# Kernel optimization log

Measured on AMD Instinct MI355X. Metric: run time of the kernel, lower is better.

## Reference

```python
import jax, jax.numpy as jnp
import numpy as np
import math

B, T, D, H = 2, 2048, 1024, 16
DH = D // H          # 64
NB = DH // 2         # 32 rope blocks
EPS = 1e-5


def _layernorm(x, g, b):
    m = jnp.mean(x, axis=-1, keepdims=True)
    v = jnp.var(x, axis=-1, keepdims=True)
    return (x - m) * jax.lax.rsqrt(v + EPS) * g + b


def _rope(x, cos, sin):
    # x: (B,H,T,DH); cos/sin: (B,H,T,NB)
    x1 = x[..., 0::2]
    x2 = x[..., 1::2]
    o1 = x1 * cos - x2 * sin
    o2 = x1 * sin + x2 * cos
    return jnp.stack([o1, o2], axis=-1).reshape(x.shape)


def setup_inputs() -> dict:
    key = jax.random.key(0)
    ks = jax.random.split(key, 16)
    x = jax.random.normal(ks[0], (B, T, D), dtype=jnp.float32)
    # genuine RoPE angles broadcast to (B,H,T,NB)
    inv_freq = 1.0 / (10000.0 ** (np.arange(NB, dtype=np.float32) / NB))
    ang = jnp.asarray(np.arange(T, dtype=np.float32)[:, None] * inv_freq[None, :])  # (T,NB)
    cos_a = jnp.broadcast_to(jnp.cos(ang)[None, None], (B, H, T, NB)).astype(jnp.float32)
    sin_a = jnp.broadcast_to(jnp.sin(ang)[None, None], (B, H, T, NB)).astype(jnp.float32)
    causal_mask = jnp.triu(jnp.ones((T, T), dtype=bool), k=1)  # True above diagonal -> masked
    s = 0.02
    def w(k, shp):
        return jax.random.normal(k, shp, dtype=jnp.float32) * s
    return {
        "x": x, "cos_a": cos_a, "sin_a": sin_a, "causal_mask": causal_mask,
        "Wq": w(ks[1], (D, D)), "bq": jnp.zeros((D,), jnp.float32),
        "Wk": w(ks[2], (D, D)), "bk": jnp.zeros((D,), jnp.float32),
        "Wv": w(ks[3], (D, D)), "bv": jnp.zeros((D,), jnp.float32),
        "Wo": w(ks[4], (D, D)), "bo": jnp.zeros((D,), jnp.float32),
        "g1": jnp.ones((D,), jnp.float32), "b1n": jnp.zeros((D,), jnp.float32),
        "g2": jnp.ones((D,), jnp.float32), "b2n": jnp.zeros((D,), jnp.float32),
        "W1": w(ks[5], (D, 4 * D)), "bf1": jnp.zeros((4 * D,), jnp.float32),
        "W2": w(ks[6], (4 * D, D)), "bf2": jnp.zeros((D,), jnp.float32),
    }


def reference(x, cos_a, sin_a, causal_mask, Wq, bq, Wk, bk, Wv, bv, Wo, bo,
              g1, b1n, g2, b2n, W1, bf1, W2, bf2):
    h = _layernorm(x, g1, b1n)
    def heads(y):
        return y.reshape(B, T, H, DH).transpose(0, 2, 1, 3)  # (B,H,T,DH)
    Q = heads(h @ Wq + bq)
    K = heads(h @ Wk + bk)
    V = heads(h @ Wv + bv)
    Q = _rope(Q, cos_a, sin_a)
    K = _rope(K, cos_a, sin_a)
    scale = math.sqrt(DH)
    scores = jnp.einsum('bhqd,bhkd->bhqk', Q, K) / scale
    scores = jnp.where(causal_mask[None, None], -jnp.inf, scores)
    attn = jax.nn.softmax(scores, axis=-1)
    out = jnp.einsum('bhqk,bhkd->bhqd', attn, V)
    out = out.transpose(0, 2, 1, 3).reshape(B, T, D)
    out = out @ Wo + bo
    x = x + out  # dropout=0.0 (eval)
    h2 = _layernorm(x, g2, b2n)
    ffn = jax.nn.gelu(h2 @ W1 + bf1, approximate=False) @ W2 + bf2
    return x + ffn
```

## Files before the change

### kernel.cpp

```cpp
#include <hip/hip_runtime.h>

typedef unsigned short u16;
typedef unsigned int   u32;
typedef __attribute__((ext_vector_type(8))) short          short8;
typedef __attribute__((ext_vector_type(4))) float          f32x4;
typedef __attribute__((ext_vector_type(8))) unsigned short u16x8;
typedef __attribute__((ext_vector_type(4))) unsigned short u16x4;

#define T_SEQ  2048
#define DMODEL 1024
#define NHEAD  16
#define DHEAD  64
#define HBUF   4194304

__device__ __forceinline__ float bf2f(u16 u) {
    u32 i = ((u32)u) << 16; float f; __builtin_memcpy(&f, &i, 4); return f;
}
__device__ __forceinline__ u16 f2bf(float f) {
    u32 x; __builtin_memcpy(&x, &f, 4);
    return (u16)((x + 0x7FFFu + ((x >> 16) & 1u)) >> 16);
}

__device__ __forceinline__ void gld16(const u16* g, u16* l) {
    auto gp = reinterpret_cast<const __attribute__((address_space(1))) u32*>(
        reinterpret_cast<uintptr_t>(g));
    auto lp = reinterpret_cast<__attribute__((address_space(3))) u32*>(
        (u32)reinterpret_cast<uintptr_t>(l));
    __builtin_amdgcn_global_load_lds(gp, lp, 16, 0, 0);
}

__global__ __launch_bounds__(256) void ln_k(const float* __restrict__ x,
                                            const float* __restrict__ g,
                                            const float* __restrict__ bb,
                                            u16* __restrict__ out)
{
    int row = blockIdx.x, tid = threadIdx.x;
    const float* xr = x + (size_t)row * DMODEL;
    f32x4 v = *(const f32x4*)(xr + tid * 4);
    float s  = v[0] + v[1] + v[2] + v[3];
    float s2 = v[0]*v[0] + v[1]*v[1] + v[2]*v[2] + v[3]*v[3];
    #pragma unroll
    for (int o = 32; o; o >>= 1) { s += __shfl_xor(s, o); s2 += __shfl_xor(s2, o); }
    __shared__ float rs[4], rq[4];
    if ((tid & 63) == 0) { rs[tid >> 6] = s; rq[tid >> 6] = s2; }
    __syncthreads();
    float S  = rs[0] + rs[1] + rs[2] + rs[3];
    float S2 = rq[0] + rq[1] + rq[2] + rq[3];
    float mean = S * (1.f / DMODEL);
    float var  = S2 * (1.f / DMODEL) - mean * mean;
    float rstd = rsqrtf(var + 1e-5f);
    f32x4 gv = *(const f32x4*)(g + tid * 4);
    f32x4 bv = *(const f32x4*)(bb + tid * 4);
    u16x4 o;
    #pragma unroll
    for (int e = 0; e < 4; e++)
        o[e] = f2bf((v[e] - mean) * rstd * gv[e] + bv[e]);
    *(u16x4*)(out + (size_t)row * DMODEL + tid * 4) = o;
}

__device__ __forceinline__ void tr_body(const float* __restrict__ in,
                                        u16* __restrict__ out, int R, int C,
                                        int bx, int by, int tid)
{
    __shared__ u16 s[64][72];
    int c0 = bx * 64, r0 = by * 64;
    #pragma unroll
    for (int p = 0; p < 2; p++) {
        int r = (tid >> 3) + p * 32, cq = (tid & 7) * 8;
        const float* ip = in + (size_t)(r0 + r) * C + c0 + cq;
        f32x4 a = *(const f32x4*)ip;
        f32x4 b = *(const f32x4*)(ip + 4);
        u16x8 o;
        #pragma unroll
        for (int e = 0; e < 4; e++) { o[e] = f2bf(a[e]); o[4 + e] = f2bf(b[e]); }
        *(u16x8*)(&s[r][cq]) = o;
    }
    __syncthreads();
    int oc = tid >> 2, kq = (tid & 3) * 16;
    u16 tmp[16] __attribute__((aligned(16)));
    #pragma unroll
    for (int e = 0; e < 16; e++) tmp[e] = s[kq + e][oc];
    u16* op = out + (size_t)(c0 + oc) * R + r0 + kq;
    *(u16x8*)op       = *(const u16x8*)(&tmp[0]);
    *(u16x8*)(op + 8) = *(const u16x8*)(&tmp[8]);
}

__global__ __launch_bounds__(256) void trall_k(const float* __restrict__ w0, const float* __restrict__ w1,
                                               const float* __restrict__ w2, const float* __restrict__ w3,
                                               const float* __restrict__ wf1, const float* __restrict__ wf2,
                                               u16* __restrict__ o0, u16* __restrict__ o1,
                                               u16* __restrict__ o2, u16* __restrict__ o3,
                                               u16* __restrict__ of1, u16* __restrict__ of2)
{
    int z = blockIdx.z;
    if (z < 4) {
        const float* in = (z == 0) ? w0 : (z == 1) ? w1 : (z == 2) ? w2 : w3;
        u16* out        = (z == 0) ? o0 : (z == 1) ? o1 : (z == 2) ? o2 : o3;
        tr_body(in, out, 1024, 1024, blockIdx.x, blockIdx.y, threadIdx.x);
    } else if (z < 8) {
        tr_body(wf1, of1, 1024, 4096, blockIdx.x + 16 * (z - 4), blockIdx.y, threadIdx.x);
    } else {
        tr_body(wf2, of2, 4096, 1024, blockIdx.x, blockIdx.y + 16 * (z - 8), threadIdx.x);
    }
}

constexpr int EPI_QKV = 0, EPI_RESF = 1, EPI_GELU = 2, EPI_RES2 = 3;

template<int EPI, int BM>
__global__ __launch_bounds__(256) void gemm_k(
    const u16* __restrict__ A, const u16* __restrict__ Bt, void* __restrict__ outv,
    int M, int N, int K, int Kld,
    const float* __restrict__ b0, const float* __restrict__ b1, const float* __restrict__ b2,
    const float* __restrict__ resid,
    const float* __restrict__ cosp, const float* __restrict__ sinp)
{
    constexpr int MI = BM / 32;
    constexpr int ASZ = BM * 32, BSZ = 128 * 32;
    __shared__ u16 As[2 * ASZ];
    __shared__ u16 Bs[2 * BSZ];
    int tid = threadIdx.x;
    int n0 = blockIdx.x * 128, m0 = blockIdx.y * BM;
    int wave = tid >> 6, lane = tid & 63, lm = lane & 15, ko = lane >> 4;
    int wm = (wave & 1) * (BM / 2), wn = (wave >> 1) * 64;
    f32x4 acc[MI][4];
    #pragma unroll
    for (int i = 0; i < MI; i++)
        #pragma unroll
        for (int j = 0; j < 4; j++) acc[i][j] = (f32x4){0.f, 0.f, 0.f, 0.f};

    int srow = wave * 16 + (lane >> 2);
    int scol = (lane & 3) * 8;
    const u16* Ag = A  + (size_t)(m0 + srow) * Kld + scol;
    const u16* Bg = Bt + (size_t)(n0 + srow) * Kld + scol;
    u16* Al = &As[wave * 16 * 32];
    u16* Bl = &Bs[wave * 16 * 32];

    gld16(Ag, Al);
    if constexpr (BM == 128) gld16(Ag + 64 * (size_t)Kld, Al + 64 * 32);
    gld16(Bg,                    Bl);
    gld16(Bg + 64 * (size_t)Kld, Bl + 64 * 32);

    int t = 0;
    for (int kt = 0; kt < K; kt += 32, t ^= 1) {
        __syncthreads();
        if (kt + 32 < K) {
            u16* Al2 = Al + (t ^ 1) * ASZ;
            u16* Bl2 = Bl + (t ^ 1) * BSZ;
            gld16(Ag + 32, Al2);
            if constexpr (BM == 128) gld16(Ag + 64 * (size_t)Kld + 32, Al2 + 64 * 32);
            gld16(Bg + 32,                    Bl2);
            gld16(Bg + 64 * (size_t)Kld + 32, Bl2 + 64 * 32);
        }
        const u16* Ab = &As[t * ASZ];
        const u16* Bb = &Bs[t * BSZ];
        short8 af[MI], bf[4];
        #pragma unroll
        for (int i = 0; i < MI; i++) af[i] = *(const short8*)(&Ab[(wm + i * 16 + lm) * 32 + ko * 8]);
        #pragma unroll
        for (int j = 0; j < 4; j++) bf[j] = *(const short8*)(&Bb[(wn + j * 16 + lm) * 32 + ko * 8]);
        #pragma unroll
        for (int i = 0; i < MI; i++)
            #pragma unroll
            for (int j = 0; j < 4; j++)
                acc[i][j] = __builtin_amdgcn_mfma_f32_16x16x32_bf16(af[i], bf[j], acc[i][j], 0, 0, 0);
        Ag += 32; Bg += 32;
    }

    #pragma unroll
    for (int i = 0; i < MI; i++) {
        #pragma unroll
        for (int j = 0; j < 4; j++) {
            int n = n0 + wn + j * 16 + lm;
            #pragma unroll
            for (int r = 0; r < 4; r++) {
                int m = m0 + wm + i * 16 + ko * 4 + r;
                float v = acc[i][j][r];
                if constexpr (EPI == EPI_QKV) {
                    int which = n >> 10, nn = n & 1023;
                    const float* bp = (which == 0) ? b0 : (which == 1 ? b1 : b2);
                    v += bp[nn];
                    float vp = __shfl_xor(v, 1);
                    int bi = m >> 11, t2 = m & 2047, hh = nn >> 6, d = nn & 63;
                    u16* outp = (u16*)outv + (size_t)which * HBUF;
                    if (which < 2) {
                        size_t oidx = ((size_t)((bi * NHEAD + hh) * T_SEQ + t2)) * DHEAD + d;
                        size_t ci = ((size_t)((bi * NHEAD + hh) * T_SEQ + t2)) * 32 + (d >> 1);
                        float c = cosp[ci], sn = sinp[ci];
                        float o = (d & 1) ? (vp * sn + v * c) : (v * c - vp * sn);
                        if (which == 0) o *= 0.18033688f;
                        outp[oidx] = f2bf(o);
                    } else {
                        size_t oidx = ((size_t)((bi * NHEAD + hh) * DHEAD + d)) * T_SEQ + t2;
                        outp[oidx] = f2bf(v);
                    }
                } else if constexpr (EPI == EPI_RESF) {
                    v += b0[n] + resid[(size_t)m * N + n];
                    ((float*)outv)[(size_t)m * N + n] = v;
                } else if constexpr (EPI == EPI_GELU) {
                    v += b0[n];
                    float gl = 0.5f * v * (1.f + erff(v * 0.70710678118654752f));
                    ((u16*)outv)[(size_t)m * N + n] = f2bf(gl);
                } else {
                    v += b0[n] + resid[(size_t)m * N + n];
                    ((float*)outv)[(size_t)m * N + n] = v;
                }
            }
        }
    }
}

__device__ __forceinline__ void attn_step(
    bool diag, int wave, int lm, int ko,
    short8 aq0, short8 aq1,
    const u16 (*sK)[72], const u16 (*sV)[72], u16 (*sPw)[72],
    f32x4* oacc, float* lr)
{
    f32x4 sacc[4];
    #pragma unroll
    for (int j = 0; j < 4; j++) {
        short8 bk0 = *(const short8*)(&sK[j * 16 + lm][ko * 8]);
        short8 bk1 = *(const short8*)(&sK[j * 16 + lm][32 + ko * 8]);
        f32x4 z = (f32x4){0.f, 0.f, 0.f, 0.f};
        z = __builtin_amdgcn_mfma_f32_16x16x32_bf16(aq0, bk0, z, 0, 0, 0);
        z = __builtin_amdgcn_mfma_f32_16x16x32_bf16(aq1, bk1, z, 0, 0, 0);
        sacc[j] = z;
    }
    if (diag) {
        #pragma unroll
        for (int j = 0; j < 4; j++)
            #pragma unroll
            for (int r = 0; r < 4; r++)
                if (j * 16 + lm > wave * 16 + ko * 4 + r) sacc[j][r] = -1e30f;
    }

    u16 pb[4][4];
    #pragma unroll
    for (int j = 0; j < 4; j++)
        #pragma unroll
        for (int r = 0; r < 4; r++) {
            float p = __builtin_amdgcn_exp2f(sacc[j][r]);
            lr[r] += p;
            pb[j][r] = f2bf(p);
        }

    #pragma unroll
    for (int j = 0; j < 4; j++)
        #pragma unroll
        for (int r = 0; r < 4; r++) sPw[ko * 4 + r][j * 16 + lm] = pb[j][r];

    #pragma unroll
    for (int ks = 0; ks < 2; ks++) {
        short8 ap = *(const short8*)(&sPw[lm][ks * 32 + ko * 8]);
        #pragma unroll
        for (int j = 0; j < 4; j++) {
            short8 bv = *(const short8*)(&sV[j * 16 + lm][ks * 32 + ko * 8]);
            oacc[j] = __builtin_amdgcn_mfma_f32_16x16x32_bf16(ap, bv, oacc[j], 0, 0, 0);
        }
    }
}

__global__ __launch_bounds__(256) void fattn_k(const u16* __restrict__ Q,
                                               const u16* __restrict__ K,
                                               const u16* __restrict__ Vt,
                                               u16* __restrict__ out)
{
    __shared__ u16 sQP[4][16][72];
    __shared__ u16 sK[2][64][72];
    __shared__ u16 sV[2][64][72];
    int tid = threadIdx.x;
    int qtA = blockIdx.x;
    int qtB = 31 - qtA;
    int bh = blockIdx.y;
    int wave = tid >> 6, lane = tid & 63, lm = lane & 15, ko = lane >> 4;
    int bi = bh >> 4, hh = bh & 15;

    const u16* Kb = K  + (size_t)bh * T_SEQ * DHEAD;
    const u16* Vb = Vt + (size_t)bh * DHEAD * T_SEQ;
    u16* sQf = &sQP[0][0][0];
    int srow = tid >> 2, scol = (tid & 3) * 16;

    short8 aqA0, aqA1, aqB0, aqB1;
    {
        const u16* QbA = Q + ((size_t)bh * T_SEQ + qtA * 64) * DHEAD + (size_t)srow * DHEAD + scol;
        *(u16x8*)(&sQf[srow * 72 + scol])     = *(const u16x8*)QbA;
        *(u16x8*)(&sQf[srow * 72 + scol + 8]) = *(const u16x8*)(QbA + 8);
        __syncthreads();
        aqA0 = *(const short8*)(&sQf[(wave * 16 + lm) * 72 + ko * 8]);
        aqA1 = *(const short8*)(&sQf[(wave * 16 + lm) * 72 + 32 + ko * 8]);
        __syncthreads();
        const u16* QbB = Q + ((size_t)bh * T_SEQ + qtB * 64) * DHEAD + (size_t)srow * DHEAD + scol;
        *(u16x8*)(&sQf[srow * 72 + scol])     = *(const u16x8*)QbB;
        *(u16x8*)(&sQf[srow * 72 + scol + 8]) = *(const u16x8*)(QbB + 8);
        __syncthreads();
        aqB0 = *(const short8*)(&sQf[(wave * 16 + lm) * 72 + ko * 8]);
        aqB1 = *(const short8*)(&sQf[(wave * 16 + lm) * 72 + 32 + ko * 8]);
    }

    f32x4 oA[4], oB[4];
    float lA[4], lB[4];
    #pragma unroll
    for (int j = 0; j < 4; j++) { oA[j] = (f32x4){0,0,0,0}; oB[j] = (f32x4){0,0,0,0}; }
    #pragma unroll
    for (int r = 0; r < 4; r++) { lA[r] = 0.f; lB[r] = 0.f; }

    int nA = qtA + 1, n = nA + qtB + 1;

    u16x8 pk0, pk1, pv0, pv1;
    {
        const u16* kp = Kb + (size_t)srow * DHEAD + scol;
        pk0 = *(const u16x8*)kp; pk1 = *(const u16x8*)(kp + 8);
        const u16* vp = Vb + (size_t)srow * T_SEQ + scol;
        pv0 = *(const u16x8*)vp; pv1 = *(const u16x8*)(vp + 8);
    }

    for (int i = 0; i < n; i++) {
        bool isA = i < nA;
        int kt = isA ? i : i - nA;
        int buf = i & 1;

        *(u16x8*)(&sK[buf][srow][scol])     = pk0;
        *(u16x8*)(&sK[buf][srow][scol + 8]) = pk1;
        *(u16x8*)(&sV[buf][srow][scol])     = pv0;
        *(u16x8*)(&sV[buf][srow][scol + 8]) = pv1;

        if (i + 1 < n) {
            int kt2 = (i + 1 < nA) ? i + 1 : i + 1 - nA;
            const u16* kp = Kb + ((size_t)(kt2 * 64 + srow)) * DHEAD + scol;
            pk0 = *(const u16x8*)kp; pk1 = *(const u16x8*)(kp + 8);
            const u16* vp = Vb + (size_t)srow * T_SEQ + kt2 * 64 + scol;
            pv0 = *(const u16x8*)vp; pv1 = *(const u16x8*)(vp + 8);
        }

        __syncthreads();

        if (isA)
            attn_step(kt == qtA, wave, lm, ko, aqA0, aqA1, sK[buf], sV[buf], sQP[wave], oA, lA);
        else
            attn_step(kt == qtB, wave, lm, ko, aqB0, aqB1, sK[buf], sV[buf], sQP[wave], oB, lB);
    }

    #pragma unroll
    for (int o = 1; o < 16; o <<= 1)
        #pragma unroll
        for (int r = 0; r < 4; r++) { lA[r] += __shfl_xor(lA[r], o); lB[r] += __shfl_xor(lB[r], o); }
    #pragma unroll
    for (int r = 0; r < 4; r++) { lA[r] = 1.f / lA[r]; lB[r] = 1.f / lB[r]; }
    int qrowA = qtA * 64 + wave * 16, qrowB = qtB * 64 + wave * 16;
    #pragma unroll
    for (int j = 0; j < 4; j++)
        #pragma unroll
        for (int r = 0; r < 4; r++) {
            out[((size_t)(bi * T_SEQ) + qrowA + ko * 4 + r) * DMODEL + hh * DHEAD + j * 16 + lm]
                = f2bf(oA[j][r] * lA[r]);
            out[((size_t)(bi * T_SEQ) + qrowB + ko * 4 + r) * DMODEL + hh * DHEAD + j * 16 + lm]
                = f2bf(oB[j][r] * lB[r]);
        }
}

extern "C" void kernel_launch(void* const* d_in, const int* in_sizes, int n_in,
                              void* d_out, int out_size, void* d_ws, size_t ws_size,
                              hipStream_t stream)
{
    (void)in_sizes; (void)n_in; (void)out_size; (void)ws_size;
    const float* x    = (const float*)d_in[0];
    const float* cosp = (const float*)d_in[1];
    const float* sinp = (const float*)d_in[2];
    const float* Wq  = (const float*)d_in[4];
    const float* bq  = (const float*)d_in[5];
    const float* Wk  = (const float*)d_in[6];
    const float* bk  = (const float*)d_in[7];
    const float* Wv  = (const float*)d_in[8];
    const float* bv  = (const float*)d_in[9];
    const float* Wo  = (const float*)d_in[10];
    const float* bo  = (const float*)d_in[11];
    const float* g1  = (const float*)d_in[12];
    const float* b1n = (const float*)d_in[13];
    const float* g2  = (const float*)d_in[14];
    const float* b2n = (const float*)d_in[15];
    const float* W1  = (const float*)d_in[16];
    const float* bf1 = (const float*)d_in[17];
    const float* W2  = (const float*)d_in[18];
    const float* bf2 = (const float*)d_in[19];

    char* ws = (char*)d_ws;
    const size_t MB = 1024 * 1024;
    u16*   qkvT  = (u16*)(ws + 0);
    u16*   WoT   = (u16*)(ws + 6 * MB);
    u16*   W1T   = (u16*)(ws + 8 * MB);
    u16*   W2T   = (u16*)(ws + 16 * MB);
    u16*   h     = (u16*)(ws + 24 * MB);
    u16*   qkvh  = (u16*)(ws + 32 * MB);
    u16*   attnC = (u16*)(ws + 56 * MB);
    float* x2    = (float*)(ws + 64 * MB);
    u16*   ffnh  = (u16*)(ws + 80 * MB);

    trall_k<<<dim3(16, 16, 12), 256, 0, stream>>>(
        Wq, Wk, Wv, Wo, W1, W2,
        qkvT, qkvT + 1 * MB, qkvT + 2 * MB, WoT, W1T, W2T);

    ln_k<<<4096, 256, 0, stream>>>(x, g1, b1n, h);
    gemm_k<EPI_QKV, 128><<<dim3(24, 32), 256, 0, stream>>>(
        h, qkvT, qkvh, 4096, 3072, 1024, 1024, bq, bk, bv, nullptr, cosp, sinp);
    fattn_k<<<dim3(16, 32), 256, 0, stream>>>(qkvh, qkvh + HBUF, qkvh + 2 * HBUF, attnC);
    gemm_k<EPI_RESF, 64><<<dim3(8, 64), 256, 0, stream>>>(
        attnC, WoT, x2, 4096, 1024, 1024, 1024, bo, nullptr, nullptr, x, nullptr, nullptr);
    ln_k<<<4096, 256, 0, stream>>>(x2, g2, b2n, h);
    gemm_k<EPI_GELU, 128><<<dim3(32, 32), 256, 0, stream>>>(
        h, W1T, ffnh, 4096, 4096, 1024, 1024, bf1, nullptr, nullptr, nullptr, nullptr, nullptr);
    gemm_k<EPI_RES2, 64><<<dim3(8, 64), 256, 0, stream>>>(
        ffnh, W2T, (float*)d_out, 4096, 1024, 4096, 4096, bf2, nullptr, nullptr, x2, nullptr, nullptr);
}
```

Before: 418.2 us.

## Replace double-buffered GEMM prefetch with load-both-then-compute 64-wide K steps

The GEMM main loop used to prefetch the next 32-wide K chunk into the second LDS buffer while computing on the current one. It now loads two 32-wide chunks into both buffers, synchronizes, then computes both, advancing K by 64 per iteration. This halves the number of loop iterations, but it adds a second barrier per iteration and removes the overlap between global loads and MFMA compute. That loss of overlap is likely to expose memory latency.

```diff
diff --git a/kernel.cpp b/kernel.cpp
--- a/kernel.cpp
+++ b/kernel.cpp
@@ -114,10 +114,11 @@
     const float* __restrict__ resid,
     const float* __restrict__ cosp, const float* __restrict__ sinp)
 {
-    constexpr int MI = BM / 32;
-    constexpr int ASZ = BM * 32, BSZ = 128 * 32;
-    __shared__ u16 As[2 * ASZ];
-    __shared__ u16 Bs[2 * BSZ];
+    constexpr int MI  = BM / 32;
+    constexpr int ACH = BM * 32;
+    constexpr int BCH = 128 * 32;
+    __shared__ u16 As[2 * ACH];
+    __shared__ u16 Bs[2 * BCH];
     int tid = threadIdx.x;
     int n0 = blockIdx.x * 128, m0 = blockIdx.y * BM;
     int wave = tid >> 6, lane = tid & 63, lm = lane & 15, ko = lane >> 4;
@@ -135,35 +136,34 @@
     u16* Al = &As[wave * 16 * 32];
     u16* Bl = &Bs[wave * 16 * 32];
 
-    gld16(Ag, Al);
-    if constexpr (BM == 128) gld16(Ag + 64 * (size_t)Kld, Al + 64 * 32);
-    gld16(Bg,                    Bl);
-    gld16(Bg + 64 * (size_t)Kld, Bl + 64 * 32);
-
-    int t = 0;
-    for (int kt = 0; kt < K; kt += 32, t ^= 1) {
-        __syncthreads();
-        if (kt + 32 < K) {
-            u16* Al2 = Al + (t ^ 1) * ASZ;
-            u16* Bl2 = Bl + (t ^ 1) * BSZ;
-            gld16(Ag + 32, Al2);
-            if constexpr (BM == 128) gld16(Ag + 64 * (size_t)Kld + 32, Al2 + 64 * 32);
-            gld16(Bg + 32,                    Bl2);
-            gld16(Bg + 64 * (size_t)Kld + 32, Bl2 + 64 * 32);
-        }
-        const u16* Ab = &As[t * ASZ];
-        const u16* Bb = &Bs[t * BSZ];
-        short8 af[MI], bf[4];
-        #pragma unroll
-        for (int i = 0; i < MI; i++) af[i] = *(const short8*)(&Ab[(wm + i * 16 + lm) * 32 + ko * 8]);
-        #pragma unroll
-        for (int j = 0; j < 4; j++) bf[j] = *(const short8*)(&Bb[(wn + j * 16 + lm) * 32 + ko * 8]);
-        #pragma unroll
-        for (int i = 0; i < MI; i++)
+    for (int kt = 0; kt < K; kt += 64) {
+        __syncthreads();
+        #pragma unroll
+        for (int c = 0; c < 2; c++) {
+            const u16* Agc = Ag + c * 32;
+            const u16* Bgc = Bg + c * 32;
+            gld16(Agc, Al + c * ACH);
+            if constexpr (BM == 128) gld16(Agc + 64 * (size_t)Kld, Al + c * ACH + 64 * 32);
+            gld16(Bgc,                    Bl + c * BCH);
+            gld16(Bgc + 64 * (size_t)Kld, Bl + c * BCH + 64 * 32);
+        }
+        Ag += 64; Bg += 64;
+        __syncthreads();
+        #pragma unroll
+        for (int c = 0; c < 2; c++) {
+            const u16* Ab = &As[c * ACH];
+            const u16* Bb = &Bs[c * BCH];
+            short8 af[MI], bf[4];
             #pragma unroll
-            for (int j = 0; j < 4; j++)
-                acc[i][j] = __builtin_amdgcn_mfma_f32_16x16x32_bf16(af[i], bf[j], acc[i][j], 0, 0, 0);
-        Ag += 32; Bg += 32;
+            for (int i = 0; i < MI; i++) af[i] = *(const short8*)(&Ab[(wm + i * 16 + lm) * 32 + ko * 8]);
+            #pragma unroll
+            for (int j = 0; j < 4; j++) bf[j] = *(const short8*)(&Bb[(wn + j * 16 + lm) * 32 + ko * 8]);
+            #pragma unroll
+            for (int i = 0; i < MI; i++)
+                #pragma unroll
+                for (int j = 0; j < 4; j++)
+                    acc[i][j] = __builtin_amdgcn_mfma_f32_16x16x32_bf16(af[i], bf[j], acc[i][j], 0, 0, 0);
+        }
     }
 
     #pragma unroll
```

After: 447.2 us. 6.9% more time.
